# Kernel tuning notes

Measured on AMD Instinct MI355X. Metric: run time of the kernel, lower is better.

The kernel has to match this reference:

```python
import jax, jax.numpy as jnp
import numpy as np

H = 16  # num_heads

def setup_inputs() -> dict:
    key = jax.random.key(0)
    ks = jax.random.split(key, 6)
    B, N, D = 2, 2048, 1024
    s = 0.02
    return {
        "x": jax.random.normal(ks[0], (B, N, D), jnp.float32),
        "attn_bias": jax.random.normal(ks[1], (B, N), jnp.float32),
        "w_qkv": jax.random.normal(ks[2], (D, 3 * D), jnp.float32) * s,
        "b_qkv": jnp.zeros((3 * D,), jnp.float32),
        "w_proj": jax.random.normal(ks[3], (D, D), jnp.float32) * s,
        "b_proj": jnp.zeros((D,), jnp.float32),
    }

def reference(x, attn_bias, w_qkv, b_qkv, w_proj, b_proj):
    B, N, D = x.shape
    hd = D // H
    qkv = x @ w_qkv + b_qkv                       # (B,N,3D)
    qkv = qkv.reshape(B, N, 3, H, hd)
    q, k, v = qkv[:, :, 0], qkv[:, :, 1], qkv[:, :, 2]  # (B,N,H,hd)
    scores = jnp.einsum("bqhd,bkhd->bhqk", q, k) / np.sqrt(hd).astype(x.dtype)
    scores = scores + attn_bias[:, None, None, :]  # key-wise bias (B,1,1,N)
    w = jax.nn.softmax(scores, axis=-1)
    out = jnp.einsum("bhqk,bkhd->bqhd", w, v).reshape(B, N, D)
    return out @ w_proj + b_proj
```

## Files before the change

### kernel.cpp

```cpp
#include <hip/hip_runtime.h>
#include <stdint.h>

typedef __attribute__((ext_vector_type(8))) short bf16x8;
typedef __attribute__((ext_vector_type(4))) short s16x4;
typedef __attribute__((ext_vector_type(4))) float f32x4;
typedef __attribute__((ext_vector_type(4))) unsigned int u32x4;

#define DEV __device__ __forceinline__

DEV unsigned short f2bf(float f) {
    unsigned u = __builtin_bit_cast(unsigned, f);
    u += 0x7FFFu + ((u >> 16) & 1u);
    return (unsigned short)(u >> 16);
}

DEV void gload_lds16(const void* g, void* l) {
    __builtin_amdgcn_global_load_lds(
        (const __attribute__((address_space(1))) unsigned int*)g,
        (__attribute__((address_space(3))) unsigned int*)l,
        16, 0, 0);
}

__global__ __launch_bounds__(256) void cvt_f32_bf16(
    const float* __restrict__ in, unsigned short* __restrict__ out, int n4) {
    int i = blockIdx.x * blockDim.x + threadIdx.x;
    if (i >= n4) return;
    const float4 v = reinterpret_cast<const float4*>(in)[i];
    s16x4 o;
    o.x = (short)f2bf(v.x); o.y = (short)f2bf(v.y);
    o.z = (short)f2bf(v.z); o.w = (short)f2bf(v.w);
    reinterpret_cast<s16x4*>(out)[i] = o;
}

__global__ __launch_bounds__(256) void transpose_w(
    const float* __restrict__ w, unsigned short* __restrict__ wt, int K, int N) {
    __shared__ unsigned short tile[64][72];
    const int k0 = blockIdx.y * 64, n0 = blockIdx.x * 64;
    const int t = threadIdx.x;
    #pragma unroll
    for (int i = 0; i < 4; ++i) {
        const int e = t + i * 256;
        const int r = e >> 4, c4 = e & 15;
        const float4 v = *reinterpret_cast<const float4*>(w + (size_t)(k0 + r) * N + n0 + c4 * 4);
        s16x4 o;
        o.x = (short)f2bf(v.x); o.y = (short)f2bf(v.y);
        o.z = (short)f2bf(v.z); o.w = (short)f2bf(v.w);
        *(s16x4*)&tile[r][c4 * 4] = o;
    }
    __syncthreads();
    #pragma unroll
    for (int i = 0; i < 4; ++i) {
        const int e = t + i * 256;
        const int rn = e >> 4, c4 = e & 15;
        s16x4 o;
        o.x = (short)tile[c4 * 4 + 0][rn];
        o.y = (short)tile[c4 * 4 + 1][rn];
        o.z = (short)tile[c4 * 4 + 2][rn];
        o.w = (short)tile[c4 * 4 + 3][rn];
        *(s16x4*)(wt + (size_t)(n0 + rn) * K + k0 + c4 * 4) = o;
    }
}

__global__ __launch_bounds__(512, 2)
void gemm256_qkv(const unsigned short* __restrict__ A,
                 const unsigned short* __restrict__ BT,
                 const float* __restrict__ bias,
                 unsigned short* __restrict__ q_out,
                 unsigned short* __restrict__ k_out,
                 unsigned short* __restrict__ v_out)
{
    constexpr int K = 1024;
    constexpr int NT = 16;
    __shared__ unsigned short lds[2][2][2][2][128][32];

    const int t = threadIdx.x;
    const int wave = t >> 6, lane = t & 63;
    const int l15 = lane & 15, l4 = lane >> 4;
    const int wr = wave >> 2, wc = wave & 3;

    const int lin = blockIdx.x;
    const int logical = (lin & 7) * 24 + (lin >> 3);
    const int bx = logical % 12, by = logical / 12;
    const int tile_m = by * 256, tile_n = bx * 256;

    const int st_row = t >> 2;
    const int st_col = ((t & 3) ^ ((t >> 3) & 3)) * 8;
    const int cswz   = (l4 ^ ((l15 >> 1) & 3)) * 8;

    f32x4 acc[8][4] = {};
    bf16x8 ra[4], rb[4];

    #define STAGE(buf, ab, half, kk, k0)                                           \
        gload_lds16(((ab) ? BT : A) +                                              \
                        (size_t)(((ab) ? tile_n : tile_m) + (half) * 128 + st_row) * K \
                        + (k0) + (kk) * 32 + st_col,                               \
                    &lds[buf][ab][half][kk][0][0] + wave * 512)
    #define READ_A(buf, kk, mq)                                                    \
        _Pragma("unroll") for (int i = 0; i < 4; ++i)                              \
            ra[i] = *(const bf16x8*)&lds[buf][0][wr][kk][((mq) * 4 + i) * 16 + l15][cswz];
    #define READ_B(buf, kk)                                                        \
        _Pragma("unroll") for (int n = 0; n < 4; ++n)                              \
            rb[n] = *(const bf16x8*)&lds[buf][1][wc >> 1][kk][(wc & 1) * 64 + n * 16 + l15][cswz];
    #define MFMA16(mq)                                                             \
        __builtin_amdgcn_s_setprio(1);                                             \
        _Pragma("unroll") for (int i = 0; i < 4; ++i)                              \
            _Pragma("unroll") for (int n = 0; n < 4; ++n)                          \
                acc[(mq) * 4 + i][n] = __builtin_amdgcn_mfma_f32_16x16x32_bf16(    \
                    ra[i], rb[n], acc[(mq) * 4 + i][n], 0, 0, 0);                  \
        __builtin_amdgcn_s_setprio(0);
    #define BAR()   __builtin_amdgcn_s_barrier()
    #define LGKM0() do { asm volatile("s_waitcnt lgkmcnt(0)" ::: "memory");        \
                         __builtin_amdgcn_sched_barrier(0); } while (0)

    STAGE(0, 1, 0, 0, 0);  STAGE(0, 1, 1, 0, 0);
    STAGE(0, 0, 0, 0, 0);  STAGE(0, 0, 1, 0, 0);
    STAGE(0, 1, 0, 1, 0);  STAGE(0, 1, 1, 1, 0);
    STAGE(0, 0, 0, 1, 0);  STAGE(0, 0, 1, 1, 0);
    STAGE(1, 1, 0, 0, 64); STAGE(1, 1, 1, 0, 64);
    STAGE(1, 0, 0, 0, 64); STAGE(1, 0, 1, 0, 64);
    STAGE(1, 1, 0, 1, 64); STAGE(1, 1, 1, 1, 64);
    asm volatile("s_waitcnt vmcnt(6)" ::: "memory");
    BAR();

    for (int kt = 0; kt < NT; ++kt) {
        const int buf = kt & 1;
        const int k0 = kt * 64;
        const bool s1 = (kt + 1 < NT);
        const bool s234 = (kt + 2 < NT);

        READ_A(buf, 0, 0); READ_B(buf, 0);
        if (s1) { STAGE(buf ^ 1, 0, 0, 1, k0 + 64); STAGE(buf ^ 1, 0, 1, 1, k0 + 64); }
        BAR(); LGKM0();
        MFMA16(0);
        BAR();

        READ_A(buf, 0, 1);
        if (s234) { STAGE(buf, 1, 0, 0, k0 + 128); STAGE(buf, 1, 1, 0, k0 + 128); }
        BAR(); LGKM0();
        MFMA16(1);
        BAR();

        READ_A(buf, 1, 0); READ_B(buf, 1);
        if (s234) { STAGE(buf, 0, 0, 0, k0 + 128); STAGE(buf, 0, 1, 0, k0 + 128); }
        BAR(); LGKM0();
        MFMA16(0);
        BAR();

        READ_A(buf, 1, 1);
        if (s234) { STAGE(buf, 1, 0, 1, k0 + 128); STAGE(buf, 1, 1, 1, k0 + 128); }
        BAR(); LGKM0();
        MFMA16(1);
        if (kt < NT - 2)       asm volatile("s_waitcnt vmcnt(6)" ::: "memory");
        else if (kt == NT - 2) asm volatile("s_waitcnt vmcnt(0)" ::: "memory");
        if (kt < NT - 1) BAR();
    }
    #undef STAGE
    #undef READ_A
    #undef READ_B
    #undef MFMA16
    #undef BAR
    #undef LGKM0

    float bcol[4];
    #pragma unroll
    for (int n = 0; n < 4; ++n) bcol[n] = bias[tile_n + wc * 64 + n * 16 + l15];

    #pragma unroll
    for (int m = 0; m < 8; ++m)
        #pragma unroll
        for (int n = 0; n < 4; ++n) {
            const int col = tile_n + wc * 64 + n * 16 + l15;
            const int which = col >> 10;
            const int hh = (col >> 6) & 15;
            const int d = col & 63;
            const int row0 = tile_m + wr * 128 + m * 16 + l4 * 4;
            const int bb = row0 >> 11, nn = row0 & 2047;
            if (which == 2) {
                const int nl = nn & 63;
                const int np = (nl & 32) | ((nl & 12) << 1) | ((nl & 16) >> 2) | (nl & 3);
                const size_t dstV = ((size_t)((bb * 16 + hh) * 64 + d)) * 2048 + (nn & ~63) + np;
                s16x4 pk;
                #pragma unroll
                for (int r = 0; r < 4; ++r) pk[r] = (short)f2bf(acc[m][n][r] + bcol[n]);
                *(s16x4*)&v_out[dstV] = pk;
            } else {
                #pragma unroll
                for (int r = 0; r < 4; ++r) {
                    const float v = acc[m][n][r] + bcol[n];
                    const size_t dst = ((size_t)((bb * 16 + hh) * 2048 + nn + r)) * 64 + d;
                    if (which == 0) q_out[dst] = f2bf(v * 0.125f);
                    else            k_out[dst] = f2bf(v);
                }
            }
        }
}

__global__ __launch_bounds__(256)
void gemm_proj(const unsigned short* __restrict__ A,
               const unsigned short* __restrict__ BT,
               const float* __restrict__ bias,
               float* __restrict__ f_out)
{
    constexpr int K = 1024, N = 1024;
    __shared__ unsigned short Abuf[128 * 64];
    __shared__ unsigned short Bbuf[64 * 64];

    const int t = threadIdx.x;
    const int wave = t >> 6, lane = t & 63;
    const int l15 = lane & 15, l4 = lane >> 4;
    const int tile_n = blockIdx.x * 64, tile_m = blockIdx.y * 128;

    const int srow = wave * 32 + (lane >> 3);
    const int brow = t >> 3;
    const int scol = (lane & 7) * 8;

    f32x4 acc[2][4] = {};

    for (int kt = 0; kt < 16; ++kt) {
        const int k0 = kt << 6;
        __syncthreads();
        #pragma unroll
        for (int c = 0; c < 4; ++c)
            gload_lds16(A + (size_t)(tile_m + srow + c * 8) * K + k0 + scol,
                        &Abuf[(wave * 32 + c * 8) * 64]);
        #pragma unroll
        for (int c = 0; c < 2; ++c)
            gload_lds16(BT + (size_t)(tile_n + brow + c * 32) * K + k0 + scol,
                        &Bbuf[(c * 32 + wave * 8) * 64]);
        asm volatile("s_waitcnt vmcnt(0)" ::: "memory");
        __syncthreads();

        bf16x8 ra[2][2], rb[4][2];
        #pragma unroll
        for (int m = 0; m < 2; ++m)
            #pragma unroll
            for (int ks = 0; ks < 2; ++ks)
                ra[m][ks] = *(const bf16x8*)&Abuf[(wave * 32 + m * 16 + l15) * 64 + ks * 32 + l4 * 8];
        #pragma unroll
        for (int n = 0; n < 4; ++n)
            #pragma unroll
            for (int ks = 0; ks < 2; ++ks)
                rb[n][ks] = *(const bf16x8*)&Bbuf[(n * 16 + l15) * 64 + ks * 32 + l4 * 8];

        #pragma unroll
        for (int m = 0; m < 2; ++m)
            #pragma unroll
            for (int n = 0; n < 4; ++n) {
                acc[m][n] = __builtin_amdgcn_mfma_f32_16x16x32_bf16(ra[m][0], rb[n][0], acc[m][n], 0, 0, 0);
                acc[m][n] = __builtin_amdgcn_mfma_f32_16x16x32_bf16(ra[m][1], rb[n][1], acc[m][n], 0, 0, 0);
            }
    }

    float bcol[4];
    #pragma unroll
    for (int n = 0; n < 4; ++n) bcol[n] = bias[tile_n + n * 16 + l15];

    #pragma unroll
    for (int m = 0; m < 2; ++m)
        #pragma unroll
        for (int n = 0; n < 4; ++n) {
            const int col = tile_n + n * 16 + l15;
            #pragma unroll
            for (int r = 0; r < 4; ++r) {
                const int row = tile_m + wave * 32 + m * 16 + l4 * 4 + r;
                f_out[(size_t)row * N + col] = acc[m][n][r] + bcol[n];
            }
        }
}

__global__ __launch_bounds__(512, 4)
void attn_kernel(const unsigned short* __restrict__ Qb,
                 const unsigned short* __restrict__ Kb,
                 const unsigned short* __restrict__ Vt,
                 const float* __restrict__ bias,
                 unsigned short* __restrict__ Ob)
{
    __shared__ __align__(16) unsigned char pool[40960];
    unsigned short (*Kf)[4096] = (unsigned short (*)[4096])(pool);
    unsigned short (*Vf)[4096] = (unsigned short (*)[4096])(pool + 16384);
    float* blds = (float*)(pool + 32768);
    float (*Oscr)[32][64] = (float (*)[32][64])(pool);
    float (*Lscr)[4][32]  = (float (*)[4][32])(pool + 32768);

    const unsigned di = blockIdx.x;
    const unsigned logical = (di & 7) * 64 + (di >> 3);
    const int qt = logical & 15;
    const int h  = (logical >> 4) & 15;
    const int b  = logical >> 8;

    const int t = threadIdx.x;
    const int wave = t >> 6, lane = t & 63;
    const int l15 = lane & 15, l4 = lane >> 4;
    const int wq = wave & 3, wk = wave >> 2;
    const int kb0 = wk * 32;
    const int xsw = (l15 & 7) << 3;

    const size_t head = ((size_t)(b * 16 + h)) * 2048 * 64;
    const unsigned short* Qh = Qb + head;
    const unsigned short* Kh = Kb + head;

    const int srow8 = wave * 8 + (lane >> 3);
    const int scol8 = 8 * ((lane & 7) ^ (lane >> 3));
    const unsigned short* Ksrc = Kh + (size_t)srow8 * 64 + scol8;
    const unsigned short* Vsrc = Vt + ((size_t)((b * 16 + h) * 64) + srow8) * 2048 + scol8;

    for (int i = t; i < 2048; i += 512) blds[i] = bias[b * 2048 + i] - 5.5451774f;

    const int qbase = qt * 128 + wq * 32;
    bf16x8 qf[2][2];
    #pragma unroll
    for (int qi = 0; qi < 2; ++qi)
        #pragma unroll
        for (int ks = 0; ks < 2; ++ks)
            qf[qi][ks] = *(const bf16x8*)(Qh + (size_t)(qbase + qi * 16 + l15) * 64 + ks * 32 + l4 * 8);

    float lsum[2] = {0.f, 0.f};
    f32x4 oacc[2][4] = {};

    gload_lds16(Ksrc, &Kf[0][wave * 512]);
    gload_lds16(Vsrc, &Vf[0][wave * 512]);
    __syncthreads();

    for (int kt = 0; kt < 32; ++kt) {
        const int key0 = kt * 64;
        const int pb = kt & 1;

        if (kt < 31) {
            gload_lds16(Ksrc + (size_t)(key0 + 64) * 64, &Kf[pb ^ 1][wave * 512]);
            gload_lds16(Vsrc + key0 + 64, &Vf[pb ^ 1][wave * 512]);
        }

        const unsigned short* Kp = Kf[pb];
        const unsigned short* Vp = Vf[pb];

        bf16x8 kfr[2][2];
        #pragma unroll
        for (int f = 0; f < 2; ++f)
            #pragma unroll
            for (int ks = 0; ks < 2; ++ks)
                kfr[f][ks] = *(const bf16x8*)&Kp[(kb0 + f * 16 + l15) * 64 + ((ks * 32 + l4 * 8) ^ xsw)];

        f32x4 bk[2];
        #pragma unroll
        for (int f = 0; f < 2; ++f)
            bk[f] = *(const f32x4*)&blds[key0 + kb0 + f * 16 + l4 * 4];

        f32x4 s[2][2];
        __builtin_amdgcn_s_setprio(1);
        #pragma unroll
        for (int qi = 0; qi < 2; ++qi)
            #pragma unroll
            for (int f = 0; f < 2; ++f) {
                f32x4 z = bk[f];
                z = __builtin_amdgcn_mfma_f32_16x16x32_bf16(kfr[f][0], qf[qi][0], z, 0, 0, 0);
                z = __builtin_amdgcn_mfma_f32_16x16x32_bf16(kfr[f][1], qf[qi][1], z, 0, 0, 0);
                s[qi][f] = z;
            }
        __builtin_amdgcn_s_setprio(0);

        bf16x8 pa[2];
        #pragma unroll
        for (int qi = 0; qi < 2; ++qi) {
            float ps = 0.f;
            u32x4 w;
            #pragma unroll
            for (int f = 0; f < 2; ++f) {
                const float p0 = __expf(s[qi][f][0]);
                const float p1 = __expf(s[qi][f][1]);
                const float p2 = __expf(s[qi][f][2]);
                const float p3 = __expf(s[qi][f][3]);
                ps += (p0 + p1) + (p2 + p3);
                unsigned w0, w1;
                asm("v_cvt_pk_bf16_f32 %0, %1, %2" : "=v"(w0) : "v"(p0), "v"(p1));
                asm("v_cvt_pk_bf16_f32 %0, %1, %2" : "=v"(w1) : "v"(p2), "v"(p3));
                w[f * 2] = w0; w[f * 2 + 1] = w1;
            }
            lsum[qi] += ps;
            pa[qi] = __builtin_bit_cast(bf16x8, w);
        }

        __builtin_amdgcn_s_setprio(1);
        #pragma unroll
        for (int df = 0; df < 4; ++df) {
            bf16x8 vf = *(const bf16x8*)&Vp[(df * 16 + l15) * 64 + ((kb0 + l4 * 8) ^ xsw)];
            oacc[0][df] = __builtin_amdgcn_mfma_f32_16x16x32_bf16(pa[0], vf, oacc[0][df], 0, 0, 0);
            oacc[1][df] = __builtin_amdgcn_mfma_f32_16x16x32_bf16(pa[1], vf, oacc[1][df], 0, 0, 0);
        }
        __builtin_amdgcn_s_setprio(0);

        __syncthreads();
    }

    #pragma unroll
    for (int qi = 0; qi < 2; ++qi) {
        lsum[qi] += __shfl_xor(lsum[qi], 16, 64);
        lsum[qi] += __shfl_xor(lsum[qi], 32, 64);
    }

    __syncthreads();
    if (lane < 16) {
        Lscr[wk][wq][lane] = lsum[0];
        Lscr[wk][wq][16 + lane] = lsum[1];
    }
    if (wk == 1) {
        #pragma unroll
        for (int qi = 0; qi < 2; ++qi)
            #pragma unroll
            for (int df = 0; df < 4; ++df)
                #pragma unroll
                for (int r = 0; r < 4; ++r)
                    Oscr[wq][qi * 16 + l4 * 4 + r][df * 16 + l15] = oacc[qi][df][r];
    }
    __syncthreads();
    if (wk == 0) {
        #pragma unroll
        for (int qi = 0; qi < 2; ++qi) {
            float inv[4];
            #pragma unroll
            for (int r = 0; r < 4; ++r) {
                const int ql = qi * 16 + l4 * 4 + r;
                inv[r] = 1.0f / (Lscr[0][wq][ql] + Lscr[1][wq][ql]);
            }
            #pragma unroll
            for (int r = 0; r < 4; ++r) {
                const int ql = qi * 16 + l4 * 4 + r;
                const int q = qbase + ql;
                #pragma unroll
                for (int df = 0; df < 4; ++df) {
                    const int d = df * 16 + l15;
                    const float v = oacc[qi][df][r] + Oscr[wq][ql][d];
                    Ob[((size_t)(b * 2048 + q)) * 1024 + h * 64 + d] = f2bf(v * inv[r]);
                }
            }
        }
    }
}

extern "C" void kernel_launch(void* const* d_in, const int* in_sizes, int n_in,
                              void* d_out, int out_size, void* d_ws, size_t ws_size,
                              hipStream_t stream) {
    const float* x      = (const float*)d_in[0];
    const float* abias  = (const float*)d_in[1];
    const float* w_qkv  = (const float*)d_in[2];
    const float* b_qkv  = (const float*)d_in[3];
    const float* w_proj = (const float*)d_in[4];
    const float* b_proj = (const float*)d_in[5];
    float* out = (float*)d_out;

    unsigned short* ws = (unsigned short*)d_ws;
    unsigned short* xb  = ws;
    unsigned short* wqT = xb  + (size_t)4096 * 1024;
    unsigned short* wpT = wqT + (size_t)3072 * 1024;
    unsigned short* qb  = wpT + (size_t)1024 * 1024;
    unsigned short* kb  = qb  + (size_t)2 * 16 * 2048 * 64;
    unsigned short* vt  = kb  + (size_t)2 * 16 * 2048 * 64;
    unsigned short* ao  = vt  + (size_t)2 * 16 * 2048 * 64;

    cvt_f32_bf16<<<4096, 256, 0, stream>>>(x, xb, 1048576);
    transpose_w<<<dim3(48, 16), 256, 0, stream>>>(w_qkv, wqT, 1024, 3072);
    transpose_w<<<dim3(16, 16), 256, 0, stream>>>(w_proj, wpT, 1024, 1024);
    gemm256_qkv<<<192, 512, 0, stream>>>(xb, wqT, b_qkv, qb, kb, vt);
    attn_kernel<<<512, 512, 0, stream>>>(qb, kb, vt, abias, ao);
    gemm_proj<<<dim3(16, 32), 256, 0, stream>>>(ao, wpT, b_proj, out);
}
```

Measured before the change: 115.6 us.

## Software-pipeline attention loop with 4-deep K/V LDS ring and QK lookahead

Replaces the double-buffered K/V tiles with a 4-slot LDS ring that prefetches two tiles ahead. The QK^T MFMA for tile kt+1 is issued before the softmax/PV work of tile kt, so score computation overlaps the exp and PV phase. The full __syncthreads is replaced by a partial vmcnt wait plus s_barrier, giving one barrier per iteration. LDS per block grows from 40 KB to 72 KB, which can lower the number of resident blocks per CU. It also keeps a second set of score registers live across the loop.

```diff
diff --git a/kernel.cpp b/kernel.cpp
--- a/kernel.cpp
+++ b/kernel.cpp
@@ -275,10 +275,10 @@
                  const float* __restrict__ bias,
                  unsigned short* __restrict__ Ob)
 {
-    __shared__ __align__(16) unsigned char pool[40960];
+    __shared__ __align__(16) unsigned char pool[73728];
     unsigned short (*Kf)[4096] = (unsigned short (*)[4096])(pool);
-    unsigned short (*Vf)[4096] = (unsigned short (*)[4096])(pool + 16384);
-    float* blds = (float*)(pool + 32768);
+    unsigned short (*Vf)[4096] = (unsigned short (*)[4096])(pool + 32768);
+    float* blds = (float*)(pool + 65536);
     float (*Oscr)[32][64] = (float (*)[32][64])(pool);
     float (*Lscr)[4][32]  = (float (*)[4][32])(pool + 32768);
 
@@ -317,79 +317,95 @@
     float lsum[2] = {0.f, 0.f};
     f32x4 oacc[2][4] = {};
 
+    #define QK_TILE(tt, sd)                                                              \
+        do {                                                                             \
+            const unsigned short* Kp_ = Kf[(tt) & 3];                                    \
+            bf16x8 kfr_[2][2];                                                           \
+            _Pragma("unroll") for (int f = 0; f < 2; ++f)                                \
+                _Pragma("unroll") for (int ks = 0; ks < 2; ++ks)                         \
+                    kfr_[f][ks] = *(const bf16x8*)&Kp_[(kb0 + f * 16 + l15) * 64 +       \
+                                                      ((ks * 32 + l4 * 8) ^ xsw)];       \
+            f32x4 bk_[2];                                                                \
+            _Pragma("unroll") for (int f = 0; f < 2; ++f)                                \
+                bk_[f] = *(const f32x4*)&blds[(tt) * 64 + kb0 + f * 16 + l4 * 4];        \
+            __builtin_amdgcn_s_setprio(1);                                               \
+            _Pragma("unroll") for (int qi = 0; qi < 2; ++qi)                             \
+                _Pragma("unroll") for (int f = 0; f < 2; ++f) {                          \
+                    f32x4 z_ = __builtin_amdgcn_mfma_f32_16x16x32_bf16(                  \
+                        kfr_[f][0], qf[qi][0], bk_[f], 0, 0, 0);                         \
+                    sd[qi][f] = __builtin_amdgcn_mfma_f32_16x16x32_bf16(                 \
+                        kfr_[f][1], qf[qi][1], z_, 0, 0, 0);                             \
+                }                                                                        \
+            __builtin_amdgcn_s_setprio(0);                                               \
+        } while (0)
+
     gload_lds16(Ksrc, &Kf[0][wave * 512]);
     gload_lds16(Vsrc, &Vf[0][wave * 512]);
-    __syncthreads();
+    gload_lds16(Ksrc + 4096, &Kf[1][wave * 512]);
+    gload_lds16(Vsrc + 64, &Vf[1][wave * 512]);
+    asm volatile("s_waitcnt vmcnt(2) lgkmcnt(0)" ::: "memory");
+    __builtin_amdgcn_s_barrier();
+    __builtin_amdgcn_sched_barrier(0);
+
+    f32x4 sp[2][2];
+    QK_TILE(0, sp);
 
     for (int kt = 0; kt < 32; ++kt) {
-        const int key0 = kt * 64;
-        const int pb = kt & 1;
-
+        if (kt < 30) {
+            gload_lds16(Ksrc + (size_t)(kt + 2) * 4096, &Kf[(kt + 2) & 3][wave * 512]);
+            gload_lds16(Vsrc + (kt + 2) * 64, &Vf[(kt + 2) & 3][wave * 512]);
+        }
+
+        f32x4 sn[2][2];
         if (kt < 31) {
-            gload_lds16(Ksrc + (size_t)(key0 + 64) * 64, &Kf[pb ^ 1][wave * 512]);
-            gload_lds16(Vsrc + key0 + 64, &Vf[pb ^ 1][wave * 512]);
-        }
-
-        const unsigned short* Kp = Kf[pb];
-        const unsigned short* Vp = Vf[pb];
-
-        bf16x8 kfr[2][2];
-        #pragma unroll
-        for (int f = 0; f < 2; ++f)
-            #pragma unroll
-            for (int ks = 0; ks < 2; ++ks)
-                kfr[f][ks] = *(const bf16x8*)&Kp[(kb0 + f * 16 + l15) * 64 + ((ks * 32 + l4 * 8) ^ xsw)];
-
-        f32x4 bk[2];
-        #pragma unroll
-        for (int f = 0; f < 2; ++f)
-            bk[f] = *(const f32x4*)&blds[key0 + kb0 + f * 16 + l4 * 4];
-
-        f32x4 s[2][2];
-        __builtin_amdgcn_s_setprio(1);
-        #pragma unroll
-        for (int qi = 0; qi < 2; ++qi)
-            #pragma unroll
-            for (int f = 0; f < 2; ++f) {
-                f32x4 z = bk[f];
-                z = __builtin_amdgcn_mfma_f32_16x16x32_bf16(kfr[f][0], qf[qi][0], z, 0, 0, 0);
-                z = __builtin_amdgcn_mfma_f32_16x16x32_bf16(kfr[f][1], qf[qi][1], z, 0, 0, 0);
-                s[qi][f] = z;
-            }
-        __builtin_amdgcn_s_setprio(0);
-
-        bf16x8 pa[2];
-        #pragma unroll
-        for (int qi = 0; qi < 2; ++qi) {
-            float ps = 0.f;
-            u32x4 w;
-            #pragma unroll
-            for (int f = 0; f < 2; ++f) {
-                const float p0 = __expf(s[qi][f][0]);
-                const float p1 = __expf(s[qi][f][1]);
-                const float p2 = __expf(s[qi][f][2]);
-                const float p3 = __expf(s[qi][f][3]);
-                ps += (p0 + p1) + (p2 + p3);
-                unsigned w0, w1;
-                asm("v_cvt_pk_bf16_f32 %0, %1, %2" : "=v"(w0) : "v"(p0), "v"(p1));
-                asm("v_cvt_pk_bf16_f32 %0, %1, %2" : "=v"(w1) : "v"(p2), "v"(p3));
-                w[f * 2] = w0; w[f * 2 + 1] = w1;
-            }
-            lsum[qi] += ps;
-            pa[qi] = __builtin_bit_cast(bf16x8, w);
-        }
-
-        __builtin_amdgcn_s_setprio(1);
-        #pragma unroll
-        for (int df = 0; df < 4; ++df) {
-            bf16x8 vf = *(const bf16x8*)&Vp[(df * 16 + l15) * 64 + ((kb0 + l4 * 8) ^ xsw)];
-            oacc[0][df] = __builtin_amdgcn_mfma_f32_16x16x32_bf16(pa[0], vf, oacc[0][df], 0, 0, 0);
-            oacc[1][df] = __builtin_amdgcn_mfma_f32_16x16x32_bf16(pa[1], vf, oacc[1][df], 0, 0, 0);
-        }
-        __builtin_amdgcn_s_setprio(0);
-
-        __syncthreads();
-    }
+            if (kt < 30) asm volatile("s_waitcnt vmcnt(2)" ::: "memory");
+            else         asm volatile("s_waitcnt vmcnt(0)" ::: "memory");
+            __builtin_amdgcn_s_barrier();
+            __builtin_amdgcn_sched_barrier(0);
+            QK_TILE(kt + 1, sn);
+        }
+
+        {
+            const unsigned short* Vp = Vf[kt & 3];
+            bf16x8 pa[2];
+            #pragma unroll
+            for (int qi = 0; qi < 2; ++qi) {
+                float ps = 0.f;
+                u32x4 w;
+                #pragma unroll
+                for (int f = 0; f < 2; ++f) {
+                    const float p0 = __expf(sp[qi][f][0]);
+                    const float p1 = __expf(sp[qi][f][1]);
+                    const float p2 = __expf(sp[qi][f][2]);
+                    const float p3 = __expf(sp[qi][f][3]);
+                    ps += (p0 + p1) + (p2 + p3);
+                    unsigned w0, w1;
+                    asm("v_cvt_pk_bf16_f32 %0, %1, %2" : "=v"(w0) : "v"(p0), "v"(p1));
+                    asm("v_cvt_pk_bf16_f32 %0, %1, %2" : "=v"(w1) : "v"(p2), "v"(p3));
+                    w[f * 2] = w0; w[f * 2 + 1] = w1;
+                }
+                lsum[qi] += ps;
+                pa[qi] = __builtin_bit_cast(bf16x8, w);
+            }
+
+            __builtin_amdgcn_s_setprio(1);
+            #pragma unroll
+            for (int df = 0; df < 4; ++df) {
+                bf16x8 vf = *(const bf16x8*)&Vp[(df * 16 + l15) * 64 + ((kb0 + l4 * 8) ^ xsw)];
+                oacc[0][df] = __builtin_amdgcn_mfma_f32_16x16x32_bf16(pa[0], vf, oacc[0][df], 0, 0, 0);
+                oacc[1][df] = __builtin_amdgcn_mfma_f32_16x16x32_bf16(pa[1], vf, oacc[1][df], 0, 0, 0);
+            }
+            __builtin_amdgcn_s_setprio(0);
+        }
+
+        if (kt < 31) {
+            #pragma unroll
+            for (int qi = 0; qi < 2; ++qi)
+                #pragma unroll
+                for (int f = 0; f < 2; ++f) sp[qi][f] = sn[qi][f];
+        }
+    }
+    #undef QK_TILE
 
     #pragma unroll
     for (int qi = 0; qi < 2; ++qi) {
```

Measured after the change: 117.1 us. Within noise of the previous version (+1.3%).
